# Kernel tuning notes

Measured on AMD Instinct MI355X. Metric: run time of the kernel, lower is better.

## Reference

```python
import jax, jax.numpy as jnp
import numpy as np


def setup_inputs() -> dict:
    key = jax.random.key(0)
    k1, k2, k3 = jax.random.split(key, 3)
    B, C, H, W = 16, 256, 48, 48
    INTER = C // 2
    x = jax.random.normal(k1, (B, C, H, W), dtype=jnp.float32)
    # nn.init.normal_(weight, std=0.01); 1x1 conv kernels stored as (out, in)
    theta_w = 0.01 * jax.random.normal(k2, (INTER, C), dtype=jnp.float32)
    phi_w = 0.01 * jax.random.normal(k3, (INTER, C), dtype=jnp.float32)
    theta_b = jnp.zeros((INTER,), dtype=jnp.float32)
    phi_b = jnp.zeros((INTER,), dtype=jnp.float32)
    return {"x": x, "theta_w": theta_w, "theta_b": theta_b, "phi_w": phi_w, "phi_b": phi_b}


def reference(x, theta_w, theta_b, phi_w, phi_b):
    b, c, h, w = x.shape
    inter = theta_w.shape[0]
    n = h * w
    # 1x1 conv == channel-wise linear projection
    theta_x = jnp.einsum('bchw,kc->bkhw', x, theta_w) + theta_b[None, :, None, None]
    phi_x = jnp.einsum('bchw,kc->bkhw', x, phi_w) + phi_b[None, :, None, None]
    q = theta_x.reshape(b, inter, n)   # [b, k, n]
    kmat = phi_x.reshape(b, inter, n)  # [b, k, n]
    g = x.reshape(b, c, n)             # [b, c, n]
    # f = theta^T @ phi : [b, n, n], scaled then softmaxed over last dim
    f = jnp.einsum('bkn,bkm->bnm', q, kmat) / jnp.sqrt(jnp.asarray(inter, x.dtype))
    f = jax.nn.softmax(f, axis=-1)
    # y = f @ g^T : [b, c, n]
    y = jnp.einsum('bnm,bcm->bcn', f, g)
    return y.reshape(b, c, h, w)
```

## Files before the change

kernel.cpp:

```cpp
#include <hip/hip_runtime.h>
#include <hip/hip_bf16.h>

#define B_SZ 16
#define C_IN 256
#define N_SP 2304
#define K_INT 128
#define NTILE 36
#define MT 32
#define MITER 72

typedef __attribute__((ext_vector_type(8))) short short8;
typedef __attribute__((ext_vector_type(4))) float f32x4;

__device__ __align__(16) short g_Wbf[2 * K_INT * C_IN];

__device__ inline unsigned pk_bf16(float a, float b) {
  float2 f; f.x = a; f.y = b;
  __hip_bfloat162 h = __float22bfloat162_rn(f);
  unsigned u;
  __builtin_memcpy(&u, &h, sizeof(u));
  return u;
}

__global__ __launch_bounds__(256) void wcvt_kernel(
    const float* __restrict__ tw, const float* __restrict__ pw)
{
  const int i = (blockIdx.x * 256 + threadIdx.x) * 4;
  float4 a = *(const float4*)(tw + i);
  float4 p = *(const float4*)(pw + i);
  uint2 ua; ua.x = pk_bf16(a.x, a.y); ua.y = pk_bf16(a.z, a.w);
  uint2 up; up.x = pk_bf16(p.x, p.y); up.y = pk_bf16(p.z, p.w);
  *(uint2*)(g_Wbf + i) = ua;
  *(uint2*)(g_Wbf + 32768 + i) = up;
}

__global__ __launch_bounds__(256) void proj_kernel(
    const float* __restrict__ x,
    const float* __restrict__ theta_b, const float* __restrict__ phi_b,
    short* __restrict__ Qt, short* __restrict__ Kt, short* __restrict__ Gbf)
{
  __shared__ short Xl[64][264];

  const int b  = blockIdx.x / NTILE;
  const int n0 = (blockIdx.x % NTILE) * 64;
  const int t  = threadIdx.x;

  {
    const float* xrow = x + ((size_t)b * C_IN + t) * N_SP + n0;
    unsigned tp[32];
#pragma unroll
    for (int i = 0; i < 16; ++i) {
      float4 v = ((const float4*)xrow)[i];
      tp[2*i]   = pk_bf16(v.x, v.y);
      tp[2*i+1] = pk_bf16(v.z, v.w);
    }
    uint4* grow = (uint4*)(Gbf + ((size_t)b * C_IN + t) * N_SP + n0);
#pragma unroll
    for (int i = 0; i < 8; ++i) {
      uint4 u; u.x = tp[4*i]; u.y = tp[4*i+1]; u.z = tp[4*i+2]; u.w = tp[4*i+3];
      grow[i] = u;
    }
#pragma unroll
    for (int j = 0; j < 32; ++j) {
      Xl[2*j][t]   = (short)tp[j];
      Xl[2*j+1][t] = (short)(tp[j] >> 16);
    }
  }
  __syncthreads();

  const int wave = t >> 6, lane = t & 63;
  const int col = lane & 15, quad = lane >> 4;

  f32x4 acc[2][2][4];
#pragma unroll
  for (int p = 0; p < 2; ++p)
#pragma unroll
    for (int kr = 0; kr < 2; ++kr)
#pragma unroll
      for (int j = 0; j < 4; ++j) {
        acc[p][kr][j][0] = 0.f; acc[p][kr][j][1] = 0.f;
        acc[p][kr][j][2] = 0.f; acc[p][kr][j][3] = 0.f;
      }

#pragma unroll
  for (int cs = 0; cs < 8; ++cs) {
    const int c0 = cs * 32;
    short8 afr[2][2];
#pragma unroll
    for (int p = 0; p < 2; ++p)
#pragma unroll
      for (int kr = 0; kr < 2; ++kr) {
        const int k = wave * 32 + kr * 16 + col;
        afr[p][kr] = *(const short8*)(g_Wbf + p * 32768 + k * C_IN + c0 + quad * 8);
      }
#pragma unroll
    for (int j = 0; j < 4; ++j) {
      short8 bfr = *(const short8*)&Xl[j * 16 + col][c0 + quad * 8];
#pragma unroll
      for (int p = 0; p < 2; ++p)
#pragma unroll
        for (int kr = 0; kr < 2; ++kr)
          acc[p][kr][j] = __builtin_amdgcn_mfma_f32_16x16x32_bf16(
              afr[p][kr], bfr, acc[p][kr][j], 0, 0, 0);
    }
  }

#pragma unroll
  for (int p = 0; p < 2; ++p) {
    const float* bias = p ? phi_b : theta_b;
    short* dst = p ? Kt : Qt;
#pragma unroll
    for (int kr = 0; kr < 2; ++kr) {
      const int k0 = wave * 32 + kr * 16 + quad * 4;
      float4 bv = *(const float4*)(bias + k0);
#pragma unroll
      for (int j = 0; j < 4; ++j) {
        const int n = n0 + j * 16 + col;
        f32x4 v = acc[p][kr][j];
        uint2 sv;
        sv.x = pk_bf16(v[0] + bv.x, v[1] + bv.y);
        sv.y = pk_bf16(v[2] + bv.z, v[3] + bv.w);
        *(uint2*)(dst + ((size_t)b * N_SP + n) * K_INT + k0) = sv;
      }
    }
  }
}

__global__ __launch_bounds__(256) void attn_kernel(
    const short* __restrict__ Qt, const short* __restrict__ Kt,
    const short* __restrict__ Gbf, float* __restrict__ out)
{
  __shared__ __align__(16) char Kl[2][8192];
  __shared__ __align__(16) short Pblob[2][4][64][8];
  __shared__ float l_lds[64];

  const int b   = blockIdx.x / NTILE;
  const int qn0 = (blockIdx.x % NTILE) * 64;
  const int t = threadIdx.x;
  const int wave = t >> 6, lane = t & 63;
  const int col = lane & 15, quad = lane >> 4;

  const short* Ktb = Kt  + (size_t)b * N_SP * K_INT;
  const short* Gb  = Gbf + (size_t)b * C_IN * N_SP;

  short8 qf[4];
  {
    const short* qb = Qt + ((size_t)b * N_SP + qn0 + wave * 16 + col) * K_INT + quad * 8;
#pragma unroll
    for (int kk = 0; kk < 4; ++kk) qf[kk] = *(const short8*)(qb + kk * 32);
  }

  f32x4 yacc[4][4];
#pragma unroll
  for (int i = 0; i < 4; ++i)
#pragma unroll
    for (int j = 0; j < 4; ++j) {
      yacc[i][j][0] = 0.f; yacc[i][j][1] = 0.f;
      yacc[i][j][2] = 0.f; yacc[i][j][3] = 0.f;
    }
  f32x4 lacc;
  lacc[0] = 0.f; lacc[1] = 0.f; lacc[2] = 0.f; lacc[3] = 0.f;

  short8 ones;
#pragma unroll
  for (int j = 0; j < 8; ++j) ones[j] = (short)0x3F80;

  const float SC2 = 0.12754859f;

  const int KW0 = (t >> 4) * 256 + ((((t & 15) ^ ((t >> 4) & 7))) << 4);
  int KR0[4];
#pragma unroll
  for (int kk = 0; kk < 4; ++kk)
    KR0[kk] = col * 256 + ((((kk << 2) + quad) ^ (col & 7)) << 4);

  const int koff = (t >> 4) * K_INT + (t & 15) * 8;
  const short* gbase = Gb + ((size_t)(wave * 64 + col)) * N_SP + quad * 8;

  short8 krA, krB;
  krA = *(const short8*)(Ktb + koff);
  krB = *(const short8*)(Ktb + 2048 + koff);
  *(short8*)(Kl[0] + KW0) = krA;
  *(short8*)(Kl[0] + KW0 + 4096) = krB;
  krA = *(const short8*)(Ktb + 4096 + koff);
  krB = *(const short8*)(Ktb + 6144 + koff);
  short8 gA[4], gB[4];
#pragma unroll
  for (int ct = 0; ct < 4; ++ct)
    gA[ct] = *(const short8*)(gbase + (size_t)ct * 16 * N_SP);
  __syncthreads();

#define SUBITER(MTV, CUR, GC, GN)                                              \
  {                                                                            \
                           \
    f32x4 s0, s1;                                                              \
    s0[0] = 0.f; s0[1] = 0.f; s0[2] = 0.f; s0[3] = 0.f;                        \
    s1[0] = 0.f; s1[1] = 0.f; s1[2] = 0.f; s1[3] = 0.f;                        \
    _Pragma("unroll")                                                          \
    for (int kk = 0; kk < 4; ++kk) {                                           \
      short8 a0 = *(const short8*)(Kl[CUR] + KR0[kk]);                         \
      s0 = __builtin_amdgcn_mfma_f32_16x16x32_bf16(a0, qf[kk], s0, 0, 0, 0);   \
      short8 a1 = *(const short8*)(Kl[CUR] + KR0[kk] + 4096);                  \
      s1 = __builtin_amdgcn_mfma_f32_16x16x32_bf16(a1, qf[kk], s1, 0, 0, 0);   \
    }                                                                          \
                    \
    unsigned u0 = pk_bf16(exp2f(s0[0] * SC2), exp2f(s0[1] * SC2));             \
    unsigned u1 = pk_bf16(exp2f(s0[2] * SC2), exp2f(s0[3] * SC2));             \
    unsigned u2 = pk_bf16(exp2f(s1[0] * SC2), exp2f(s1[1] * SC2));             \
    unsigned u3 = pk_bf16(exp2f(s1[2] * SC2), exp2f(s1[3] * SC2));             \
    asm("v_permlane32_swap_b32 %0, %1" : "+v"(u0), "+v"(u2));                  \
    asm("v_permlane32_swap_b32 %0, %1" : "+v"(u1), "+v"(u3));                  \
    asm("v_permlane16_swap_b32 %0, %1" : "+v"(u0), "+v"(u2));                  \
    asm("v_permlane16_swap_b32 %0, %1" : "+v"(u1), "+v"(u3));                  \
    unsigned uu[4] = {u0, u1, u2, u3};                                         \
    short8 pa; __builtin_memcpy(&pa, uu, 16);                                  \
    lacc = __builtin_amdgcn_mfma_f32_16x16x32_bf16(pa, ones, lacc, 0, 0, 0);   \
                         \
    *(short8*)&Pblob[CUR][wave][lane][0] = pa;                                 \
           \
    if ((MTV) + 1 < MITER) {                                                   \
      *(short8*)(Kl[(CUR) ^ 1] + KW0) = krA;                                   \
      *(short8*)(Kl[(CUR) ^ 1] + KW0 + 4096) = krB;                            \
    }                                                                          \
                      \
    if ((MTV) + 2 < MITER) {                                                   \
      const short* kp = Ktb + (size_t)((MTV) + 2) * 4096 + koff;               \
      krA = *(const short8*)(kp);                                              \
      krB = *(const short8*)(kp + 2048);                                       \
    }                                                                          \
               \
    if ((MTV) + 1 < MITER) {                                                   \
      _Pragma("unroll")                                                        \
      for (int ct = 0; ct < 4; ++ct)                                           \
        GN[ct] = *(const short8*)(gbase + (size_t)ct * 16 * N_SP +             \
                                  ((MTV) + 1) * 32);                           \
    }                                                                          \
    __syncthreads();                                                           \
        \
    _Pragma("unroll")                                                          \
    for (int qt = 0; qt < 4; ++qt) {                                           \
      short8 paq = *(const short8*)&Pblob[CUR][qt][lane][0];                   \
      _Pragma("unroll")                                                        \
      for (int ct = 0; ct < 4; ++ct)                                           \
        yacc[qt][ct] = __builtin_amdgcn_mfma_f32_16x16x32_bf16(                \
            paq, GC[ct], yacc[qt][ct], 0, 0, 0);                               \
    }                                                                          \
  }

  for (int mt2 = 0; mt2 < MITER / 2; ++mt2) {
    SUBITER(2 * mt2,     0, gA, gB)
    SUBITER(2 * mt2 + 1, 1, gB, gA)
  }
#undef SUBITER

  if (col == 0) {
#pragma unroll
    for (int r = 0; r < 4; ++r) l_lds[wave * 16 + quad * 4 + r] = lacc[r];
  }
  __syncthreads();

#pragma unroll
  for (int qt = 0; qt < 4; ++qt) {
    float4 lq = *(const float4*)&l_lds[qt * 16 + quad * 4];
    float4 iv;
    iv.x = 1.0f / lq.x; iv.y = 1.0f / lq.y; iv.z = 1.0f / lq.z; iv.w = 1.0f / lq.w;
    const int nb = qn0 + qt * 16 + quad * 4;
#pragma unroll
    for (int ct = 0; ct < 4; ++ct) {
      const int c = wave * 64 + ct * 16 + col;
      f32x4 v = yacc[qt][ct];
      float4 o;
      o.x = v[0] * iv.x; o.y = v[1] * iv.y; o.z = v[2] * iv.z; o.w = v[3] * iv.w;
      *(float4*)(out + ((size_t)b * C_IN + c) * N_SP + nb) = o;
    }
  }
}

extern "C" void kernel_launch(void* const* d_in, const int* in_sizes, int n_in,
                              void* d_out, int out_size, void* d_ws, size_t ws_size,
                              hipStream_t stream) {
  const float* x  = (const float*)d_in[0];
  const float* tw = (const float*)d_in[1];
  const float* tb = (const float*)d_in[2];
  const float* pw = (const float*)d_in[3];
  const float* pb = (const float*)d_in[4];
  float* out = (float*)d_out;

  short* Qt  = (short*)d_ws;
  short* Kt  = Qt + (size_t)B_SZ * N_SP * K_INT;
  short* Gbf = Kt + (size_t)B_SZ * N_SP * K_INT;

  wcvt_kernel<<<32, 256, 0, stream>>>(tw, pw);
  proj_kernel<<<B_SZ * NTILE, 256, 0, stream>>>(x, tb, pb, Qt, Kt, Gbf);
  attn_kernel<<<B_SZ * NTILE, 256, 0, stream>>>(Qt, Kt, Gbf, out);
}
```

Baseline: 245.3 us.

## Split attention into 32-query, 2-wave workgroups with XCD-aware block mapping

The attention kernel now runs 128-thread workgroups that each own 32 queries, and each wave covers 128 output channels instead of 64. The grid doubles to 1152 blocks, launch bounds request 3 workgroups per CU, and block ids are remapped so that consecutive ids land on different XCDs while neighbouring tiles of a batch stay on the same one. The G operand is no longer double-buffered; it is reloaded after the PV MFMAs. The aim is better occupancy and L2 locality, at the cost of reading K twice as often per query and having a longer exposed G-load latency.

```diff
diff --git a/kernel.cpp b/kernel.cpp
--- a/kernel.cpp
+++ b/kernel.cpp
@@ -6,6 +6,7 @@
 #define N_SP 2304
 #define K_INT 128
 #define NTILE 36
+#define NTILE2 72
 #define MT 32
 #define MITER 72
 
@@ -126,16 +127,17 @@
   }
 }
 
-__global__ __launch_bounds__(256) void attn_kernel(
+__global__ __launch_bounds__(128, 3) void attn_kernel(
     const short* __restrict__ Qt, const short* __restrict__ Kt,
     const short* __restrict__ Gbf, float* __restrict__ out)
 {
   __shared__ __align__(16) char Kl[2][8192];
-  __shared__ __align__(16) short Pblob[2][4][64][8];
-  __shared__ float l_lds[64];
-
-  const int b   = blockIdx.x / NTILE;
-  const int qn0 = (blockIdx.x % NTILE) * 64;
+  __shared__ __align__(16) short Pblob[2][2][64][8];
+  __shared__ float l_lds[32];
+
+  const int wg  = (blockIdx.x & 7) * 144 + (blockIdx.x >> 3);
+  const int b   = wg / NTILE2;
+  const int qn0 = (wg % NTILE2) * 32;
   const int t = threadIdx.x;
   const int wave = t >> 6, lane = t & 63;
   const int col = lane & 15, quad = lane >> 4;
@@ -150,11 +152,11 @@
     for (int kk = 0; kk < 4; ++kk) qf[kk] = *(const short8*)(qb + kk * 32);
   }
 
-  f32x4 yacc[4][4];
-#pragma unroll
-  for (int i = 0; i < 4; ++i)
-#pragma unroll
-    for (int j = 0; j < 4; ++j) {
+  f32x4 yacc[2][8];
+#pragma unroll
+  for (int i = 0; i < 2; ++i)
+#pragma unroll
+    for (int j = 0; j < 8; ++j) {
       yacc[i][j][0] = 0.f; yacc[i][j][1] = 0.f;
       yacc[i][j][2] = 0.f; yacc[i][j][3] = 0.f;
     }
@@ -167,29 +169,29 @@
 
   const float SC2 = 0.12754859f;
 
-  const int KW0 = (t >> 4) * 256 + ((((t & 15) ^ ((t >> 4) & 7))) << 4);
+  const int KW = (t >> 4) * 256 + ((((t & 15) ^ ((t >> 4) & 7))) << 4);
   int KR0[4];
 #pragma unroll
   for (int kk = 0; kk < 4; ++kk)
     KR0[kk] = col * 256 + ((((kk << 2) + quad) ^ (col & 7)) << 4);
 
-  const int koff = (t >> 4) * K_INT + (t & 15) * 8;
-  const short* gbase = Gb + ((size_t)(wave * 64 + col)) * N_SP + quad * 8;
-
-  short8 krA, krB;
-  krA = *(const short8*)(Ktb + koff);
-  krB = *(const short8*)(Ktb + 2048 + koff);
-  *(short8*)(Kl[0] + KW0) = krA;
-  *(short8*)(Kl[0] + KW0 + 4096) = krB;
-  krA = *(const short8*)(Ktb + 4096 + koff);
-  krB = *(const short8*)(Ktb + 6144 + koff);
-  short8 gA[4], gB[4];
-#pragma unroll
-  for (int ct = 0; ct < 4; ++ct)
-    gA[ct] = *(const short8*)(gbase + (size_t)ct * 16 * N_SP);
+  const int KG = (t >> 4) * K_INT + (t & 15) * 8;
+  const short* gbase = Gb + ((size_t)(wave * 128 + col)) * N_SP + quad * 8;
+
+  short8 kr[4];
+#pragma unroll
+  for (int i = 0; i < 4; ++i) kr[i] = *(const short8*)(Ktb + KG + i * 1024);
+#pragma unroll
+  for (int i = 0; i < 4; ++i) *(short8*)(Kl[0] + KW + i * 2048) = kr[i];
+#pragma unroll
+  for (int i = 0; i < 4; ++i) kr[i] = *(const short8*)(Ktb + 4096 + KG + i * 1024);
+  short8 g[8];
+#pragma unroll
+  for (int ct = 0; ct < 8; ++ct)
+    g[ct] = *(const short8*)(gbase + (size_t)ct * 16 * N_SP);
   __syncthreads();
 
-#define SUBITER(MTV, CUR, GC, GN)                                              \
+#define SUBITER(MTV, CUR)                                                      \
   {                                                                            \
                            \
     f32x4 s0, s1;                                                              \
@@ -216,39 +218,40 @@
     lacc = __builtin_amdgcn_mfma_f32_16x16x32_bf16(pa, ones, lacc, 0, 0, 0);   \
                          \
     *(short8*)&Pblob[CUR][wave][lane][0] = pa;                                 \
-           \
+                 \
     if ((MTV) + 1 < MITER) {                                                   \
-      *(short8*)(Kl[(CUR) ^ 1] + KW0) = krA;                                   \
-      *(short8*)(Kl[(CUR) ^ 1] + KW0 + 4096) = krB;                            \
+      _Pragma("unroll")                                                        \
+      for (int i = 0; i < 4; ++i)                                              \
+        *(short8*)(Kl[(CUR) ^ 1] + KW + i * 2048) = kr[i];                     \
     }                                                                          \
                       \
     if ((MTV) + 2 < MITER) {                                                   \
-      const short* kp = Ktb + (size_t)((MTV) + 2) * 4096 + koff;               \
-      krA = *(const short8*)(kp);                                              \
-      krB = *(const short8*)(kp + 2048);                                       \
-    }                                                                          \
-               \
+      const short* kp = Ktb + (size_t)((MTV) + 2) * 4096 + KG;                 \
+      _Pragma("unroll")                                                        \
+      for (int i = 0; i < 4; ++i) kr[i] = *(const short8*)(kp + i * 1024);     \
+    }                                                                          \
+    __syncthreads();                                                           \
+             \
+    _Pragma("unroll")                                                          \
+    for (int qt = 0; qt < 2; ++qt) {                                           \
+      short8 paq = *(const short8*)&Pblob[CUR][qt][lane][0];                   \
+      _Pragma("unroll")                                                        \
+      for (int ct = 0; ct < 8; ++ct)                                           \
+        yacc[qt][ct] = __builtin_amdgcn_mfma_f32_16x16x32_bf16(                \
+            paq, g[ct], yacc[qt][ct], 0, 0, 0);                                \
+    }                                                                          \
+             \
     if ((MTV) + 1 < MITER) {                                                   \
       _Pragma("unroll")                                                        \
-      for (int ct = 0; ct < 4; ++ct)                                           \
-        GN[ct] = *(const short8*)(gbase + (size_t)ct * 16 * N_SP +             \
-                                  ((MTV) + 1) * 32);                           \
-    }                                                                          \
-    __syncthreads();                                                           \
-        \
-    _Pragma("unroll")                                                          \
-    for (int qt = 0; qt < 4; ++qt) {                                           \
-      short8 paq = *(const short8*)&Pblob[CUR][qt][lane][0];                   \
-      _Pragma("unroll")                                                        \
-      for (int ct = 0; ct < 4; ++ct)                                           \
-        yacc[qt][ct] = __builtin_amdgcn_mfma_f32_16x16x32_bf16(                \
-            paq, GC[ct], yacc[qt][ct], 0, 0, 0);                               \
+      for (int ct = 0; ct < 8; ++ct)                                           \
+        g[ct] = *(const short8*)(gbase + (size_t)ct * 16 * N_SP +              \
+                                 ((MTV) + 1) * 32);                            \
     }                                                                          \
   }
 
   for (int mt2 = 0; mt2 < MITER / 2; ++mt2) {
-    SUBITER(2 * mt2,     0, gA, gB)
-    SUBITER(2 * mt2 + 1, 1, gB, gA)
+    SUBITER(2 * mt2,     0)
+    SUBITER(2 * mt2 + 1, 1)
   }
 #undef SUBITER
 
@@ -259,14 +262,14 @@
   __syncthreads();
 
 #pragma unroll
-  for (int qt = 0; qt < 4; ++qt) {
+  for (int qt = 0; qt < 2; ++qt) {
     float4 lq = *(const float4*)&l_lds[qt * 16 + quad * 4];
     float4 iv;
     iv.x = 1.0f / lq.x; iv.y = 1.0f / lq.y; iv.z = 1.0f / lq.z; iv.w = 1.0f / lq.w;
     const int nb = qn0 + qt * 16 + quad * 4;
 #pragma unroll
-    for (int ct = 0; ct < 4; ++ct) {
-      const int c = wave * 64 + ct * 16 + col;
+    for (int ct = 0; ct < 8; ++ct) {
+      const int c = wave * 128 + ct * 16 + col;
       f32x4 v = yacc[qt][ct];
       float4 o;
       o.x = v[0] * iv.x; o.y = v[1] * iv.y; o.z = v[2] * iv.z; o.w = v[3] * iv.w;
@@ -291,5 +294,5 @@
 
   wcvt_kernel<<<32, 256, 0, stream>>>(tw, pw);
   proj_kernel<<<B_SZ * NTILE, 256, 0, stream>>>(x, tb, pb, Qt, Kt, Gbf);
-  attn_kernel<<<B_SZ * NTILE, 256, 0, stream>>>(Qt, Kt, Gbf, out);
-}
+  attn_kernel<<<B_SZ * NTILE2, 128, 0, stream>>>(Qt, Kt, Gbf, out);
+}
```

After: 358.5 us. 1.46x slower.

## Coalesce projection input loads with swizzled LDS, remap attention blocks, move barrier earlier

Applied to the files above, without the earlier changes.

The projection kernel now has threads read x so that consecutive threads cover consecutive spatial positions, giving coalesced float4 loads and uint2 stores. It writes the bf16 tile into LDS using an XOR swizzle on the channel index to avoid bank conflicts, and the MFMA fragment reads apply the matching swizzle. The attention kernel remaps block IDs so that consecutive blocks are spread across batches, which is probably meant to balance L2/XCD locality. Its barrier now sits before the global K/G prefetch loads rather than after them, which changes how load latency overlaps with synchronization.

```diff
diff --git a/kernel.cpp b/kernel.cpp
--- a/kernel.cpp
+++ b/kernel.cpp
@@ -46,30 +46,30 @@
   const int t  = threadIdx.x;
 
   {
-    const float* xrow = x + ((size_t)b * C_IN + t) * N_SP + n0;
-    unsigned tp[32];
+    const int cr = t >> 4;
+    const int a  = t & 15;
+    const int n  = a * 4;
+    const int g8 = (a & 3) << 3;
+    const float* xs = x + ((size_t)b * C_IN + cr) * N_SP + n0 + n;
+    short* gs = Gbf + ((size_t)b * C_IN + cr) * N_SP + n0 + n;
 #pragma unroll
     for (int i = 0; i < 16; ++i) {
-      float4 v = ((const float4*)xrow)[i];
-      tp[2*i]   = pk_bf16(v.x, v.y);
-      tp[2*i+1] = pk_bf16(v.z, v.w);
-    }
-    uint4* grow = (uint4*)(Gbf + ((size_t)b * C_IN + t) * N_SP + n0);
-#pragma unroll
-    for (int i = 0; i < 8; ++i) {
-      uint4 u; u.x = tp[4*i]; u.y = tp[4*i+1]; u.z = tp[4*i+2]; u.w = tp[4*i+3];
-      grow[i] = u;
-    }
-#pragma unroll
-    for (int j = 0; j < 32; ++j) {
-      Xl[2*j][t]   = (short)tp[j];
-      Xl[2*j+1][t] = (short)(tp[j] >> 16);
+      float4 v = *(const float4*)(xs + (size_t)i * 16 * N_SP);
+      unsigned p0 = pk_bf16(v.x, v.y), p1 = pk_bf16(v.z, v.w);
+      uint2 u; u.x = p0; u.y = p1;
+      *(uint2*)(gs + (size_t)i * 16 * N_SP) = u;
+      const int cs0 = (cr + 16 * i) ^ g8;
+      Xl[n + 0][cs0] = (short)p0;
+      Xl[n + 1][cs0] = (short)(p0 >> 16);
+      Xl[n + 2][cs0] = (short)p1;
+      Xl[n + 3][cs0] = (short)(p1 >> 16);
     }
   }
   __syncthreads();
 
   const int wave = t >> 6, lane = t & 63;
   const int col = lane & 15, quad = lane >> 4;
+  const int rg8 = ((col >> 2) & 3) << 3;
 
   f32x4 acc[2][2][4];
 #pragma unroll
@@ -95,7 +95,7 @@
       }
 #pragma unroll
     for (int j = 0; j < 4; ++j) {
-      short8 bfr = *(const short8*)&Xl[j * 16 + col][c0 + quad * 8];
+      short8 bfr = *(const short8*)&Xl[j * 16 + col][(c0 + quad * 8) ^ rg8];
 #pragma unroll
       for (int p = 0; p < 2; ++p)
 #pragma unroll
@@ -134,8 +134,9 @@
   __shared__ __align__(16) short Pblob[2][4][64][8];
   __shared__ float l_lds[64];
 
-  const int b   = blockIdx.x / NTILE;
-  const int qn0 = (blockIdx.x % NTILE) * 64;
+  const int wg  = (blockIdx.x & 7) * 72 + (blockIdx.x >> 3);
+  const int b   = wg / NTILE;
+  const int qn0 = (wg % NTILE) * 64;
   const int t = threadIdx.x;
   const int wave = t >> 6, lane = t & 63;
   const int col = lane & 15, quad = lane >> 4;
@@ -167,7 +168,7 @@
 
   const float SC2 = 0.12754859f;
 
-  const int KW0 = (t >> 4) * 256 + ((((t & 15) ^ ((t >> 4) & 7))) << 4);
+  const int KW = (t >> 4) * 256 + ((((t & 15) ^ ((t >> 4) & 7))) << 4);
   int KR0[4];
 #pragma unroll
   for (int kk = 0; kk < 4; ++kk)
@@ -179,8 +180,8 @@
   short8 krA, krB;
   krA = *(const short8*)(Ktb + koff);
   krB = *(const short8*)(Ktb + 2048 + koff);
-  *(short8*)(Kl[0] + KW0) = krA;
-  *(short8*)(Kl[0] + KW0 + 4096) = krB;
+  *(short8*)(Kl[0] + KW) = krA;
+  *(short8*)(Kl[0] + KW + 4096) = krB;
   krA = *(const short8*)(Ktb + 4096 + koff);
   krB = *(const short8*)(Ktb + 6144 + koff);
   short8 gA[4], gB[4];
@@ -216,26 +217,26 @@
     lacc = __builtin_amdgcn_mfma_f32_16x16x32_bf16(pa, ones, lacc, 0, 0, 0);   \
                          \
     *(short8*)&Pblob[CUR][wave][lane][0] = pa;                                 \
-           \
+        \
     if ((MTV) + 1 < MITER) {                                                   \
-      *(short8*)(Kl[(CUR) ^ 1] + KW0) = krA;                                   \
-      *(short8*)(Kl[(CUR) ^ 1] + KW0 + 4096) = krB;                            \
-    }                                                                          \
-                      \
+      *(short8*)(Kl[(CUR) ^ 1] + KW) = krA;                                    \
+      *(short8*)(Kl[(CUR) ^ 1] + KW + 4096) = krB;                             \
+    }                                                                          \
+    __syncthreads();                                                           \
+        \
     if ((MTV) + 2 < MITER) {                                                   \
       const short* kp = Ktb + (size_t)((MTV) + 2) * 4096 + koff;               \
       krA = *(const short8*)(kp);                                              \
       krB = *(const short8*)(kp + 2048);                                       \
     }                                                                          \
-               \
+          \
     if ((MTV) + 1 < MITER) {                                                   \
       _Pragma("unroll")                                                        \
       for (int ct = 0; ct < 4; ++ct)                                           \
         GN[ct] = *(const short8*)(gbase + (size_t)ct * 16 * N_SP +             \
                                   ((MTV) + 1) * 32);                           \
     }                                                                          \
-    __syncthreads();                                                           \
-        \
+             \
     _Pragma("unroll")                                                          \
     for (int qt = 0; qt < 4; ++qt) {                                           \
       short8 paq = *(const short8*)&Pblob[CUR][qt][lane][0];                   \
```

Measured after the change: 263.7 us. 7.5% more time.

## Coalesce projection kernel loads/stores with swizzled LDS staging and weight prefetch

Applied to the files above, without the earlier changes.

The projection kernel now reads x with each thread covering 4 channels by 4 positions, which gives coalesced float4 loads and Gbf stores. The transposed bf16 tile is written into an XOR-swizzled LDS buffer to avoid bank conflicts. Weight fragments are double-buffered so the next channel slice is prefetched while the current MFMAs run. Q/K outputs are staged through LDS and written as full 16-byte row segments instead of scattered 8-byte stores, at the cost of extra barriers.

```diff
diff --git a/kernel.cpp b/kernel.cpp
--- a/kernel.cpp
+++ b/kernel.cpp
@@ -39,37 +39,60 @@
     const float* __restrict__ theta_b, const float* __restrict__ phi_b,
     short* __restrict__ Qt, short* __restrict__ Kt, short* __restrict__ Gbf)
 {
-  __shared__ short Xl[64][264];
+  __shared__ __align__(16) char Xs[32768];
 
   const int b  = blockIdx.x / NTILE;
   const int n0 = (blockIdx.x % NTILE) * 64;
   const int t  = threadIdx.x;
-
-  {
-    const float* xrow = x + ((size_t)b * C_IN + t) * N_SP + n0;
-    unsigned tp[32];
-#pragma unroll
-    for (int i = 0; i < 16; ++i) {
-      float4 v = ((const float4*)xrow)[i];
-      tp[2*i]   = pk_bf16(v.x, v.y);
-      tp[2*i+1] = pk_bf16(v.z, v.w);
-    }
-    uint4* grow = (uint4*)(Gbf + ((size_t)b * C_IN + t) * N_SP + n0);
-#pragma unroll
-    for (int i = 0; i < 8; ++i) {
-      uint4 u; u.x = tp[4*i]; u.y = tp[4*i+1]; u.z = tp[4*i+2]; u.w = tp[4*i+3];
-      grow[i] = u;
-    }
-#pragma unroll
-    for (int j = 0; j < 32; ++j) {
-      Xl[2*j][t]   = (short)tp[j];
-      Xl[2*j+1][t] = (short)(tp[j] >> 16);
-    }
-  }
-  __syncthreads();
-
   const int wave = t >> 6, lane = t & 63;
   const int col = lane & 15, quad = lane >> 4;
+
+  short8 afr[2][2][2];
+#pragma unroll
+  for (int p = 0; p < 2; ++p)
+#pragma unroll
+    for (int kr = 0; kr < 2; ++kr) {
+      const int k = wave * 32 + kr * 16 + col;
+      afr[0][p][kr] = *(const short8*)(g_Wbf + p * 32768 + k * C_IN + quad * 8);
+    }
+
+  {
+    const int tq = t >> 4;
+    const int a  = t & 15;
+    const float* xs = x + ((size_t)b * C_IN + tq * 4) * N_SP + n0 + a * 4;
+    short* gs = Gbf + ((size_t)b * C_IN + tq * 4) * N_SP + n0 + a * 4;
+#pragma unroll
+    for (int s = 0; s < 4; ++s) {
+      unsigned us[4][2];
+#pragma unroll
+      for (int r = 0; r < 4; ++r) {
+        float4 v = *(const float4*)(xs + ((size_t)s * 64 + r) * N_SP);
+        us[r][0] = pk_bf16(v.x, v.y);
+        us[r][1] = pk_bf16(v.z, v.w);
+        uint2 u; u.x = us[r][0]; u.y = us[r][1];
+        *(uint2*)(gs + ((size_t)s * 64 + r) * N_SP) = u;
+      }
+      const int chunk = 8 * s + (tq >> 1);
+      const int half8 = (tq & 1) * 8;
+#pragma unroll
+      for (int j = 0; j < 4; ++j) {
+        const int w = j >> 1;
+        unsigned w0, w1;
+        if ((j & 1) == 0) {
+          w0 = (us[0][w] & 0xffffu) | (us[1][w] << 16);
+          w1 = (us[2][w] & 0xffffu) | (us[3][w] << 16);
+        } else {
+          w0 = (us[0][w] >> 16) | (us[1][w] & 0xffff0000u);
+          w1 = (us[2][w] >> 16) | (us[3][w] & 0xffff0000u);
+        }
+        const int n = 4 * a + j;
+        const int msk = (n ^ a) & 7;
+        uint2 u; u.x = w0; u.y = w1;
+        *(uint2*)(Xs + n * 512 + ((chunk ^ msk) << 4) + half8) = u;
+      }
+    }
+  }
+  __syncthreads();
 
   f32x4 acc[2][2][4];
 #pragma unroll
@@ -82,47 +105,83 @@
         acc[p][kr][j][2] = 0.f; acc[p][kr][j][3] = 0.f;
       }
 
+  int rmsk[4];
+#pragma unroll
+  for (int j = 0; j < 4; ++j) {
+    const int n = 16 * j + col;
+    rmsk[j] = (n ^ (n >> 2)) & 7;
+  }
+
 #pragma unroll
   for (int cs = 0; cs < 8; ++cs) {
-    const int c0 = cs * 32;
-    short8 afr[2][2];
-#pragma unroll
-    for (int p = 0; p < 2; ++p)
-#pragma unroll
-      for (int kr = 0; kr < 2; ++kr) {
-        const int k = wave * 32 + kr * 16 + col;
-        afr[p][kr] = *(const short8*)(g_Wbf + p * 32768 + k * C_IN + c0 + quad * 8);
-      }
+    const int cur = cs & 1, nxt = cur ^ 1;
+    if (cs + 1 < 8) {
+      const int c0n = (cs + 1) * 32;
+#pragma unroll
+      for (int p = 0; p < 2; ++p)
+#pragma unroll
+        for (int kr = 0; kr < 2; ++kr) {
+          const int k = wave * 32 + kr * 16 + col;
+          afr[nxt][p][kr] =
+              *(const short8*)(g_Wbf + p * 32768 + k * C_IN + c0n + quad * 8);
+        }
+    }
 #pragma unroll
     for (int j = 0; j < 4; ++j) {
-      short8 bfr = *(const short8*)&Xl[j * 16 + col][c0 + quad * 8];
+      const int chunk = 4 * cs + quad;
+      short8 bfr = *(const short8*)(Xs + (16 * j + col) * 512 +
+                                    ((chunk ^ rmsk[j]) << 4));
 #pragma unroll
       for (int p = 0; p < 2; ++p)
 #pragma unroll
         for (int kr = 0; kr < 2; ++kr)
           acc[p][kr][j] = __builtin_amdgcn_mfma_f32_16x16x32_bf16(
-              afr[p][kr], bfr, acc[p][kr][j], 0, 0, 0);
-    }
-  }
-
+              afr[cur][p][kr], bfr, acc[p][kr][j], 0, 0, 0);
+    }
+  }
+  __syncthreads();
+
+  short* PB = (short*)Xs;
 #pragma unroll
   for (int p = 0; p < 2; ++p) {
     const float* bias = p ? phi_b : theta_b;
-    short* dst = p ? Kt : Qt;
+    short* dst0 = p ? Kt : Qt;
 #pragma unroll
     for (int kr = 0; kr < 2; ++kr) {
       const int k0 = wave * 32 + kr * 16 + quad * 4;
       float4 bv = *(const float4*)(bias + k0);
+      const int g = wave * 8 + kr * 4 + quad;
 #pragma unroll
       for (int j = 0; j < 4; ++j) {
-        const int n = n0 + j * 16 + col;
+        const int nloc = j * 16 + col;
         f32x4 v = acc[p][kr][j];
         uint2 sv;
         sv.x = pk_bf16(v[0] + bv.x, v[1] + bv.y);
         sv.y = pk_bf16(v[2] + bv.z, v[3] + bv.w);
-        *(uint2*)(dst + ((size_t)b * N_SP + n) * K_INT + k0) = sv;
-      }
-    }
+        const int gp = g ^ (nloc & 7) ^ (((nloc >> 3) & 1) << 3);
+        *(uint2*)(PB + nloc * 128 + gp * 4) = sv;
+      }
+    }
+    __syncthreads();
+    {
+      const int nloc = t >> 2, kseg = t & 3;
+      const int xb = ((nloc >> 3) & 1) << 3;
+      uint2 r8[8];
+#pragma unroll
+      for (int i = 0; i < 8; ++i) {
+        const int gp = (kseg * 8 + i) ^ (nloc & 7) ^ xb;
+        r8[i] = *(const uint2*)(PB + nloc * 128 + gp * 4);
+      }
+      short* dst = dst0 + ((size_t)b * N_SP + n0 + nloc) * K_INT + kseg * 32;
+#pragma unroll
+      for (int i2 = 0; i2 < 4; ++i2) {
+        uint4 u;
+        u.x = r8[2 * i2].x;     u.y = r8[2 * i2].y;
+        u.z = r8[2 * i2 + 1].x; u.w = r8[2 * i2 + 1].y;
+        *(uint4*)(dst + i2 * 8) = u;
+      }
+    }
+    __syncthreads();
   }
 }
 
@@ -167,7 +226,7 @@
 
   const float SC2 = 0.12754859f;
 
-  const int KW0 = (t >> 4) * 256 + ((((t & 15) ^ ((t >> 4) & 7))) << 4);
+  const int KW = (t >> 4) * 256 + ((((t & 15) ^ ((t >> 4) & 7))) << 4);
   int KR0[4];
 #pragma unroll
   for (int kk = 0; kk < 4; ++kk)
@@ -179,8 +238,8 @@
   short8 krA, krB;
   krA = *(const short8*)(Ktb + koff);
   krB = *(const short8*)(Ktb + 2048 + koff);
-  *(short8*)(Kl[0] + KW0) = krA;
-  *(short8*)(Kl[0] + KW0 + 4096) = krB;
+  *(short8*)(Kl[0] + KW) = krA;
+  *(short8*)(Kl[0] + KW + 4096) = krB;
   krA = *(const short8*)(Ktb + 4096 + koff);
   krB = *(const short8*)(Ktb + 6144 + koff);
   short8 gA[4], gB[4];
@@ -216,10 +275,10 @@
     lacc = __builtin_amdgcn_mfma_f32_16x16x32_bf16(pa, ones, lacc, 0, 0, 0);   \
                          \
     *(short8*)&Pblob[CUR][wave][lane][0] = pa;                                 \
-           \
+        \
     if ((MTV) + 1 < MITER) {                                                   \
-      *(short8*)(Kl[(CUR) ^ 1] + KW0) = krA;                                   \
-      *(short8*)(Kl[(CUR) ^ 1] + KW0 + 4096) = krB;                            \
+      *(short8*)(Kl[(CUR) ^ 1] + KW) = krA;                                    \
+      *(short8*)(Kl[(CUR) ^ 1] + KW + 4096) = krB;                             \
     }                                                                          \
                       \
     if ((MTV) + 2 < MITER) {                                                   \
@@ -235,7 +294,7 @@
                                   ((MTV) + 1) * 32);                           \
     }                                                                          \
     __syncthreads();                                                           \
-        \
+             \
     _Pragma("unroll")                                                          \
     for (int qt = 0; qt < 4; ++qt) {                                           \
       short8 paq = *(const short8*)&Pblob[CUR][qt][lane][0];                   \
```

Measured after the change: 240.3 us, median of 2. 2.1% less time.
